# Optimization experiments

Measured on AMD Instinct MI355X. Metric: run time of the kernel, lower is better.

Reference implementation:

```python
import jax, jax.numpy as jnp
import numpy as np

SCALE = 16
N_CLASSES = 7
IGNORE = -1
MIN_RATIO = 0.75


def setup_inputs() -> dict:
    key = jax.random.key(0)
    # values in [-1, 6]: -1 is the ignore label, 0..6 are classes
    label = jax.random.randint(key, (8, 1024, 1024), 0, N_CLASSES + 1, dtype=jnp.int32) - 1
    return {"label": label}


def reference(label) -> jnp.ndarray:
    bs, H, W = label.shape
    th, tw = H // SCALE, W // SCALE
    # map ignore -> extra class index n_classes
    lab = jnp.where(label == IGNORE, N_CLASSES, label)
    # one-hot [bs, H, W, C+1]; avg_pool2d(kernel=SCALE) == blockwise mean
    oh = jax.nn.one_hot(lab, N_CLASSES + 1, dtype=jnp.float32)
    ratios = oh.reshape(bs, th, SCALE, tw, SCALE, N_CLASSES + 1).mean(axis=(2, 4))  # [bs,th,tw,C+1]
    max_ratio = ratios.max(axis=-1)                      # [bs,th,tw]
    out = ratios.argmax(axis=-1).astype(jnp.int32)       # first-max index, matches torch.max
    out = jnp.where((out == N_CLASSES) | (max_ratio < MIN_RATIO), IGNORE, out)
    return out[:, None, :, :]                            # [bs,1,th,tw]
```

## Files before the change

### kernel.cpp

```cpp
#include <hip/hip_runtime.h>


#define B_ 8
#define H_ 1024
#define W_ 1024
#define TH_ 64
#define TW_ 64

__global__ __launch_bounds__(256) void downscale_label_kernel(
    const int* __restrict__ label, int* __restrict__ out) {
  const int lane = threadIdx.x & 63;
  const int wave = threadIdx.x >> 6;
  const int p = blockIdx.x * 4 + wave;
  const int tw = p & (TW_ - 1);
  const int th = (p >> 6) & (TH_ - 1);
  const int b  = p >> 12;

  const int row = th * 16 + (lane >> 2);
  const int col = tw * 16 + ((lane & 3) << 2);
  const int4 v = *reinterpret_cast<const int4*>(
      label + ((size_t)(b * H_ + row) * W_ + col));

  unsigned long long lo = 0ull, hi = 0ull;
  int vals[4] = {v.x, v.y, v.z, v.w};
#pragma unroll
  for (int j = 0; j < 4; ++j) {
    const int cls = vals[j] & 7;
    const unsigned long long inc = 1ull << ((cls & 3) << 4);
    if (cls & 4) hi += inc; else lo += inc;
  }

#pragma unroll
  for (int s = 1; s < 64; s <<= 1) {
    lo += __shfl_xor(lo, s, 64);
    hi += __shfl_xor(hi, s, 64);
  }

  if (lane == 0) {
    int best = 0;
    int bc = (int)(lo & 0xFFFF);
#pragma unroll
    for (int c = 1; c < 8; ++c) {
      const unsigned long long src = (c < 4) ? lo : hi;
      const int cnt = (int)((src >> ((c & 3) << 4)) & 0xFFFF);
      if (cnt > bc) { bc = cnt; best = c; }
    }
    out[p] = (best == 7 || bc < 192) ? -1 : best;
  }
}

extern "C" void kernel_launch(void* const* d_in, const int* in_sizes, int n_in,
                              void* d_out, int out_size, void* d_ws, size_t ws_size,
                              hipStream_t stream) {
  const int* label = (const int*)d_in[0];
  int* out = (int*)d_out;
  const int n_pixels = B_ * TH_ * TW_;
  const int blocks = n_pixels / 4;
  downscale_label_kernel<<<blocks, 256, 0, stream>>>(label, out);
}
```

Baseline: 75.19 us.

## Assign one block per output row with threads looping over sixteen input rows

Work is remapped so each block handles one output tile row (16 input rows by 1024 columns), and each thread loops over 16 rows of int4 loads instead of one wave reducing one 16x16 tile. The full 64-lane shuffle reduction shrinks to a 4-lane reduction and one lane in four writes output. Each wave now reads contiguous 1 KB row segments, which gives more bytes in flight per thread and more coalesced access. The cost is far fewer blocks (512 instead of 8192), which may leave the GPU underfilled when hiding memory latency.

```diff
diff --git a/kernel.cpp b/kernel.cpp
--- a/kernel.cpp
+++ b/kernel.cpp
@@ -9,34 +9,34 @@
 
 __global__ __launch_bounds__(256) void downscale_label_kernel(
     const int* __restrict__ label, int* __restrict__ out) {
-  const int lane = threadIdx.x & 63;
-  const int wave = threadIdx.x >> 6;
-  const int p = blockIdx.x * 4 + wave;
-  const int tw = p & (TW_ - 1);
-  const int th = (p >> 6) & (TH_ - 1);
-  const int b  = p >> 12;
+  const int t = threadIdx.x;
+  const int bid = blockIdx.x;
+  const int b = bid >> 6;
+  const int th = bid & 63;
 
-  const int row = th * 16 + (lane >> 2);
-  const int col = tw * 16 + ((lane & 3) << 2);
-  const int4 v = *reinterpret_cast<const int4*>(
-      label + ((size_t)(b * H_ + row) * W_ + col));
+  const size_t base = ((size_t)(b * H_ + th * 16)) * W_ + (size_t)t * 4;
+  const int4* p = reinterpret_cast<const int4*>(label + base);
 
   unsigned long long lo = 0ull, hi = 0ull;
-  int vals[4] = {v.x, v.y, v.z, v.w};
 #pragma unroll
-  for (int j = 0; j < 4; ++j) {
-    const int cls = vals[j] & 7;
-    const unsigned long long inc = 1ull << ((cls & 3) << 4);
-    if (cls & 4) hi += inc; else lo += inc;
+  for (int r = 0; r < 16; ++r) {
+    const int4 v = p[r * (W_ / 4)];
+    const int vals[4] = {v.x, v.y, v.z, v.w};
+#pragma unroll
+    for (int j = 0; j < 4; ++j) {
+      const int cls = vals[j] & 7;
+      const unsigned long long inc = 1ull << ((cls & 3) << 4);
+      if (cls & 4) hi += inc; else lo += inc;
+    }
   }
 
 #pragma unroll
-  for (int s = 1; s < 64; s <<= 1) {
+  for (int s = 1; s < 4; s <<= 1) {
     lo += __shfl_xor(lo, s, 64);
     hi += __shfl_xor(hi, s, 64);
   }
 
-  if (lane == 0) {
+  if ((t & 3) == 0) {
     int best = 0;
     int bc = (int)(lo & 0xFFFF);
 #pragma unroll
@@ -45,7 +45,7 @@
       const int cnt = (int)((src >> ((c & 3) << 4)) & 0xFFFF);
       if (cnt > bc) { bc = cnt; best = c; }
     }
-    out[p] = (best == 7 || bc < 192) ? -1 : best;
+    out[bid * TW_ + (t >> 2)] = (best == 7 || bc < 192) ? -1 : best;
   }
 }
 
@@ -54,7 +54,5 @@
                               hipStream_t stream) {
   const int* label = (const int*)d_in[0];
   int* out = (int*)d_out;
-  const int n_pixels = B_ * TH_ * TW_;
-  const int blocks = n_pixels / 4;
-  downscale_label_kernel<<<blocks, 256, 0, stream>>>(label, out);
+  downscale_label_kernel<<<B_ * TH_, 256, 0, stream>>>(label, out);
 }
```

Result: faster. 70.30 us (-6.5%).
